# Kernel tuning notes

Hardware: AMD Instinct MI355X
Metric: run time of the kernel (lower is better)

## Reference

```python
import jax, jax.numpy as jnp
import numpy as np

DIM = 1024
NUM_HEADS = 16


def setup_inputs() -> dict:
    key = jax.random.key(0)
    ks = jax.random.split(key, 7)
    B, N, C = 2, 2048, DIM
    s = 1.0 / np.sqrt(C)
    x = jax.random.normal(ks[0], (B, N, C), dtype=jnp.float32)
    Wq = jax.random.normal(ks[1], (C, C), dtype=jnp.float32) * s
    Wk = jax.random.normal(ks[2], (C, C), dtype=jnp.float32) * s
    Wv = jax.random.normal(ks[3], (C, C), dtype=jnp.float32) * s
    bq = jnp.zeros((C,), dtype=jnp.float32)
    bk = jnp.zeros((C,), dtype=jnp.float32)
    bv = jnp.zeros((C,), dtype=jnp.float32)
    return {"x": x, "Wq": Wq, "bq": bq, "Wk": Wk, "bk": bk, "Wv": Wv, "bv": bv}


def reference(x, Wq, bq, Wk, bk, Wv, bv):
    B, N, C = x.shape
    H = NUM_HEADS
    D = C // H
    # Linear projections (torch Linear: x @ W.T + b)
    q = (x @ Wq.T + bq).reshape(B, N, H, D).transpose(0, 2, 1, 3)  # [B,H,N,D]
    k = (x @ Wk.T + bk).reshape(B, N, H, D).transpose(0, 2, 1, 3)
    v = (x @ Wv.T + bv).reshape(B, N, H, D).transpose(0, 2, 1, 3)
    # NOTE: original scales by sqrt(dim)=sqrt(C), not sqrt(head_dim)
    scale = 1.0 / np.sqrt(C).astype(np.float32)
    logits = jnp.einsum('bhnd,bhmd->bhnm', q, k) * scale  # [B,H,N,N]
    attn = jax.nn.softmax(logits, axis=-1)
    out = jnp.einsum('bhnm,bhmd->bhnd', attn, v)  # [B,H,N,D]
    return out.transpose(0, 2, 1, 3).reshape(B, N, C)
```

## Files before the change

kernel.cpp:

```cpp
#include <hip/hip_runtime.h>

typedef __attribute__((ext_vector_type(8))) short bf16x8;
typedef __attribute__((ext_vector_type(4))) float f32x4;
typedef __attribute__((ext_vector_type(16))) float f32x16;
typedef __attribute__((ext_vector_type(8))) unsigned short us8;
typedef unsigned short u16;
typedef unsigned int u32;

__device__ inline u16 f2bf(float f) {
  union { float f; unsigned u; } v; v.f = f;
  unsigned r = v.u + 0x7FFFu + ((v.u >> 16) & 1u);
  return (u16)(r >> 16);
}

__device__ inline u32 cvtpk_bf16(float lo, float hi) {
  u32 r;
  asm volatile("v_cvt_pk_bf16_f32 %0, %1, %2" : "=v"(r) : "v"(lo), "v"(hi));
  return r;
}

__device__ inline void gload_lds16(const void* g, void* l) {
  __builtin_amdgcn_global_load_lds(
      (const __attribute__((address_space(1))) void*)g,
      (__attribute__((address_space(3))) void*)l, 16, 0, 0);
}

__global__ void cvt_all(const float* __restrict__ x, const float* __restrict__ wq,
                        const float* __restrict__ wk, const float* __restrict__ wv,
                        u16* __restrict__ out) {
  int i = (blockIdx.x * blockDim.x + threadIdx.x) * 4;
  const float* src; int off;
  if (i < 4194304)      { src = x;  off = 0; }
  else if (i < 5242880) { src = wq; off = 4194304; }
  else if (i < 6291456) { src = wk; off = 5242880; }
  else                  { src = wv; off = 6291456; }
  float4 v = *reinterpret_cast<const float4*>(src + (i - off));
  ushort4 o;
  o.x = f2bf(v.x); o.y = f2bf(v.y); o.z = f2bf(v.z); o.w = f2bf(v.w);
  *reinterpret_cast<ushort4*>(out + i) = o;
}

__global__ __launch_bounds__(256, 3) void gemm_qkv(
    const u16* __restrict__ X,
    const u16* __restrict__ Wq, const u16* __restrict__ Wk, const u16* __restrict__ Wv,
    const float* __restrict__ bq, const float* __restrict__ bk, const float* __restrict__ bv,
    u16* __restrict__ Oq, u16* __restrict__ Ok, u16* __restrict__ Ov)
{
  constexpr int GK = 1024;
  __shared__ __align__(16) u16 As[128 * 64];
  __shared__ __align__(16) u16 Bs[128 * 64];

  const int z = blockIdx.z;
  const u16* W = (z == 0) ? Wq : (z == 1) ? Wk : Wv;
  const float* bias = (z == 0) ? bq : (z == 1) ? bk : bv;
  u16* O = (z == 0) ? Oq : (z == 1) ? Ok : Ov;
  const float scale = (z == 0) ? (1.4426950408889634f / 32.0f) : 1.0f;

  const int tid = threadIdx.x;
  const int lane = tid & 63, w = tid >> 6;
  const int wm = w >> 1, wn = w & 1;
  const int q = lane & 15, g = lane >> 4;
  const int bm0 = blockIdx.x * 128, bn0 = blockIdx.y * 128;

  int srow[4], sgc[4];
  #pragma unroll
  for (int i = 0; i < 4; ++i) {
    int c = i * 256 + tid;
    srow[i] = c >> 3;
    sgc[i] = (((c & 7) ^ ((c >> 3) & 7)) * 8);
  }

  f32x4 acc[4][4];
  #pragma unroll
  for (int i = 0; i < 4; ++i)
    #pragma unroll
    for (int j = 0; j < 4; ++j) acc[i][j] = (f32x4){0.f, 0.f, 0.f, 0.f};

  for (int k0 = 0; k0 < GK; k0 += 64) {
    #pragma unroll
    for (int i = 0; i < 4; ++i) {
      int c8 = (i * 256 + tid) * 8;
      gload_lds16(&X[(bm0 + srow[i]) * GK + k0 + sgc[i]], &As[c8]);
      gload_lds16(&W[(bn0 + srow[i]) * GK + k0 + sgc[i]], &Bs[c8]);
    }
    __syncthreads();

    #pragma unroll
    for (int kk = 0; kk < 2; ++kk) {
      bf16x8 af[4], bfr[4];
      #pragma unroll
      for (int mi = 0; mi < 4; ++mi) {
        int row = wm * 64 + mi * 16 + q;
        af[mi] = *reinterpret_cast<const bf16x8*>(
            &As[row * 64 + (((kk * 4 + g) ^ (row & 7)) * 8)]);
      }
      #pragma unroll
      for (int ni = 0; ni < 4; ++ni) {
        int row = wn * 64 + ni * 16 + q;
        bfr[ni] = *reinterpret_cast<const bf16x8*>(
            &Bs[row * 64 + (((kk * 4 + g) ^ (row & 7)) * 8)]);
      }
      #pragma unroll
      for (int mi = 0; mi < 4; ++mi)
        #pragma unroll
        for (int ni = 0; ni < 4; ++ni)
          acc[mi][ni] = __builtin_amdgcn_mfma_f32_16x16x32_bf16(af[mi], bfr[ni], acc[mi][ni], 0, 0, 0);
    }
    __syncthreads();
  }

  #pragma unroll
  for (int mi = 0; mi < 4; ++mi) {
    #pragma unroll
    for (int ni = 0; ni < 4; ++ni) {
      int col = bn0 + wn * 64 + ni * 16 + q;
      float bb = bias[col];
      int h = col >> 6, d = col & 63;
      #pragma unroll
      for (int r = 0; r < 4; ++r) {
        int row = bm0 + wm * 64 + mi * 16 + 4 * g + r;
        int b = row >> 11, n = row & 2047;
        float v = (acc[mi][ni][r] + bb) * scale;
        O[(((b << 4) + h) * 2048 + n) * 64 + d] = f2bf(v);
      }
    }
  }
}

__global__ __launch_bounds__(256) void vt_kernel(const u16* __restrict__ V, u16* __restrict__ Vt) {
  __shared__ u16 T[64 * 66];
  const int bh = blockIdx.y, n0 = blockIdx.x * 64;
  const int tid = threadIdx.x;
  #pragma unroll
  for (int i = 0; i < 2; ++i) {
    int c = i * 256 + tid;
    int n = c >> 3, col = (c & 7) * 8;
    us8 v = *reinterpret_cast<const us8*>(&V[(bh * 2048 + n0 + n) * 64 + col]);
    #pragma unroll
    for (int j = 0; j < 8; ++j) T[n * 66 + col + j] = v[j];
  }
  __syncthreads();
  #pragma unroll
  for (int i = 0; i < 2; ++i) {
    int c = i * 256 + tid;
    int d = c >> 3, nc = (c & 7) * 8;
    us8 o;
    #pragma unroll
    for (int j = 0; j < 8; ++j) o[j] = T[(nc + j) * 66 + d];
    *reinterpret_cast<us8*>(&Vt[(bh * 64 + d) * 2048 + n0 + nc]) = o;
  }
}

__global__ __launch_bounds__(512, 4) void attn_kernel(
    const u16* __restrict__ Q, const u16* __restrict__ K, const u16* __restrict__ Vt,
    float* __restrict__ out)
{
  __shared__ __align__(16) u16 smem[32768];
  u16* Kbase = smem;
  u16* Vbase = smem + 16384;

  const int tid = threadIdx.x;
  const int lane = tid & 63, w = tid >> 6;
  const int half = w >> 2, w4 = w & 3;
  const int tid256 = w4 * 64 + lane;
  const int ql = lane & 31, h = lane >> 5, l7 = lane & 7;

  const int lin = blockIdx.x;
  const int xcd = lin & 7, li = lin >> 3;
  const int bh = xcd * 4 + (li >> 4);
  const int b = bh >> 4, hd = bh & 15;
  const int qrow0 = (li & 15) * 128 + w4 * 32;

  const u16* Qp = Q + (bh * 2048 + qrow0 + ql) * 64;
  const u16* Kp = K + (bh * 2048 + half * 1024) * 64;
  const u16* Vp = Vt + bh * 64 * 2048 + half * 1024;

  bf16x8 qf[4];
  #pragma unroll
  for (int ks = 0; ks < 4; ++ks)
    qf[ks] = *reinterpret_cast<const bf16x8*>(Qp + 16 * ks + 8 * h);

  int krow_i[2], kcolb_i[2];
  #pragma unroll
  for (int i = 0; i < 2; ++i) {
    int c = i * 256 + tid256;
    krow_i[i] = c >> 3;
    kcolb_i[i] = 16 * ((c & 7) ^ ((c >> 3) & 7));
  }

  f32x16 o0, o1;
  #pragma unroll
  for (int i = 0; i < 16; ++i) { o0[i] = 0.0f; o1[i] = 0.0f; }
  float lsum = 0.0f;

  u16* Kh = Kbase + half * 8192;
  u16* Vh = Vbase + half * 8192;

  {
    #pragma unroll
    for (int i = 0; i < 2; ++i) {
      gload_lds16((const char*)(Kp + krow_i[i] * 64) + kcolb_i[i],
                  &Kh[i * 2048 + w4 * 512]);
      gload_lds16((const char*)(Vp + krow_i[i] * 2048) + kcolb_i[i],
                  &Vh[i * 2048 + w4 * 512]);
    }
    __syncthreads();
  }

  for (int t = 0; t < 16; ++t) {
    const int cur = t & 1, nxt = cur ^ 1;
    const int kb = t * 64;
    if (t < 15) {
      const int kbn = kb + 64;
      #pragma unroll
      for (int i = 0; i < 2; ++i) {
        gload_lds16((const char*)(Kp + (kbn + krow_i[i]) * 64) + kcolb_i[i],
                    &Kh[nxt * 4096 + i * 2048 + w4 * 512]);
        gload_lds16((const char*)(Vp + krow_i[i] * 2048 + kbn) + kcolb_i[i],
                    &Vh[nxt * 4096 + i * 2048 + w4 * 512]);
      }
    }

    f32x16 p0, p1;
    #pragma unroll
    for (int i = 0; i < 16; ++i) { p0[i] = 0.0f; p1[i] = 0.0f; }
    const u16* kl = Kh + cur * 4096;
    __builtin_amdgcn_s_setprio(1);
    #pragma unroll
    for (int ks = 0; ks < 4; ++ks) {
      int cb = (16 * ks + 8 * h) ^ (l7 << 3);
      bf16x8 kf0 = *reinterpret_cast<const bf16x8*>(kl + ql * 64 + cb);
      p0 = __builtin_amdgcn_mfma_f32_32x32x16_bf16(kf0, qf[ks], p0, 0, 0, 0);
      bf16x8 kf1 = *reinterpret_cast<const bf16x8*>(kl + (32 + ql) * 64 + cb);
      p1 = __builtin_amdgcn_mfma_f32_32x32x16_bf16(kf1, qf[ks], p1, 0, 0, 0);
    }
    __builtin_amdgcn_s_setprio(0);

    #pragma unroll
    for (int i = 0; i < 16; ++i) {
      p0[i] = __builtin_amdgcn_exp2f(p0[i]);
      p1[i] = __builtin_amdgcn_exp2f(p1[i]);
    }
    float sa[8];
    #pragma unroll
    for (int i = 0; i < 8; ++i)
      sa[i] = (p0[i] + p0[i + 8]) + (p1[i] + p1[i + 8]);
    float rs = ((sa[0] + sa[1]) + (sa[2] + sa[3])) + ((sa[4] + sa[5]) + (sa[6] + sa[7]));
    rs += __shfl_xor(rs, 32);
    lsum += rs;

    bf16x8 pf[4];
    {
      union { u32 u[4]; bf16x8 v; } fr;
      u32 a0 = cvtpk_bf16(p0[0], p0[1]),   c0 = cvtpk_bf16(p0[2], p0[3]);
      u32 b0 = cvtpk_bf16(p0[4], p0[5]),   d0 = cvtpk_bf16(p0[6], p0[7]);
      asm volatile("v_permlane32_swap_b32 %0, %1" : "+v"(a0), "+v"(b0));
      asm volatile("v_permlane32_swap_b32 %0, %1" : "+v"(c0), "+v"(d0));
      fr.u[0] = a0; fr.u[1] = c0; fr.u[2] = b0; fr.u[3] = d0;  pf[0] = fr.v;
      u32 a1 = cvtpk_bf16(p0[8], p0[9]),   c1 = cvtpk_bf16(p0[10], p0[11]);
      u32 b1 = cvtpk_bf16(p0[12], p0[13]), d1 = cvtpk_bf16(p0[14], p0[15]);
      asm volatile("v_permlane32_swap_b32 %0, %1" : "+v"(a1), "+v"(b1));
      asm volatile("v_permlane32_swap_b32 %0, %1" : "+v"(c1), "+v"(d1));
      fr.u[0] = a1; fr.u[1] = c1; fr.u[2] = b1; fr.u[3] = d1;  pf[1] = fr.v;
      u32 a2 = cvtpk_bf16(p1[0], p1[1]),   c2 = cvtpk_bf16(p1[2], p1[3]);
      u32 b2 = cvtpk_bf16(p1[4], p1[5]),   d2 = cvtpk_bf16(p1[6], p1[7]);
      asm volatile("v_permlane32_swap_b32 %0, %1" : "+v"(a2), "+v"(b2));
      asm volatile("v_permlane32_swap_b32 %0, %1" : "+v"(c2), "+v"(d2));
      fr.u[0] = a2; fr.u[1] = c2; fr.u[2] = b2; fr.u[3] = d2;  pf[2] = fr.v;
      u32 a3 = cvtpk_bf16(p1[8], p1[9]),   c3 = cvtpk_bf16(p1[10], p1[11]);
      u32 b3 = cvtpk_bf16(p1[12], p1[13]), d3 = cvtpk_bf16(p1[14], p1[15]);
      asm volatile("v_permlane32_swap_b32 %0, %1" : "+v"(a3), "+v"(b3));
      asm volatile("v_permlane32_swap_b32 %0, %1" : "+v"(c3), "+v"(d3));
      fr.u[0] = a3; fr.u[1] = c3; fr.u[2] = b3; fr.u[3] = d3;  pf[3] = fr.v;
    }

    const u16* vl = Vh + cur * 4096;
    __builtin_amdgcn_s_setprio(1);
    #pragma unroll
    for (int f = 0; f < 4; ++f) {
      int cb = (16 * f + 8 * h) ^ (l7 << 3);
      bf16x8 vf0 = *reinterpret_cast<const bf16x8*>(vl + ql * 64 + cb);
      o0 = __builtin_amdgcn_mfma_f32_32x32x16_bf16(vf0, pf[f], o0, 0, 0, 0);
      bf16x8 vf1 = *reinterpret_cast<const bf16x8*>(vl + (32 + ql) * 64 + cb);
      o1 = __builtin_amdgcn_mfma_f32_32x32x16_bf16(vf1, pf[f], o1, 0, 0, 0);
    }
    __builtin_amdgcn_s_setprio(0);

    __syncthreads();
  }

  float* Of = reinterpret_cast<float*>(smem);
  float* Lf = Of + 4 * 64 * 33;
  const int obase = (w4 * 64 + lane) * 33;
  if (half == 1) {
    #pragma unroll
    for (int i = 0; i < 16; ++i) { Of[obase + i] = o0[i]; Of[obase + 16 + i] = o1[i]; }
    Lf[w4 * 64 + lane] = lsum;
  }
  __syncthreads();
  if (half == 0) {
    #pragma unroll
    for (int i = 0; i < 16; ++i) { o0[i] += Of[obase + i]; o1[i] += Of[obase + 16 + i]; }
    lsum += Lf[w4 * 64 + lane];

    float r = 1.0f / lsum;
    float* op = out + ((size_t)(b * 2048 + qrow0 + ql) * 1024 + hd * 64);
    #pragma unroll
    for (int g2 = 0; g2 < 4; ++g2) {
      float4 v0, v1;
      v0.x = o0[4 * g2 + 0] * r; v0.y = o0[4 * g2 + 1] * r;
      v0.z = o0[4 * g2 + 2] * r; v0.w = o0[4 * g2 + 3] * r;
      v1.x = o1[4 * g2 + 0] * r; v1.y = o1[4 * g2 + 1] * r;
      v1.z = o1[4 * g2 + 2] * r; v1.w = o1[4 * g2 + 3] * r;
      *reinterpret_cast<float4*>(op + 8 * g2 + 4 * h)      = v0;
      *reinterpret_cast<float4*>(op + 32 + 8 * g2 + 4 * h) = v1;
    }
  }
}

extern "C" void kernel_launch(void* const* d_in, const int* in_sizes, int n_in,
                              void* d_out, int out_size, void* d_ws, size_t ws_size,
                              hipStream_t stream) {
  const float* x  = (const float*)d_in[0];
  const float* Wq = (const float*)d_in[1];
  const float* bq = (const float*)d_in[2];
  const float* Wk = (const float*)d_in[3];
  const float* bk = (const float*)d_in[4];
  const float* Wv = (const float*)d_in[5];
  const float* bv = (const float*)d_in[6];
  float* out = (float*)d_out;

  u16* ws  = (u16*)d_ws;
  u16* xb  = ws;
  u16* wqb = xb  + 4194304;
  u16* wkb = wqb + 1048576;
  u16* wvb = wkb + 1048576;
  u16* qb  = wvb + 1048576;
  u16* kb  = qb  + 4194304;
  u16* vb  = kb  + 4194304;
  u16* vt  = xb;

  cvt_all<<<7168, 256, 0, stream>>>(x, Wq, Wk, Wv, ws);

  gemm_qkv<<<dim3(32, 8, 3), 256, 0, stream>>>(xb, wqb, wkb, wvb, bq, bk, bv, qb, kb, vb);

  vt_kernel<<<dim3(32, 32), 256, 0, stream>>>(vb, vt);

  attn_kernel<<<512, 512, 0, stream>>>(qb, kb, vt, out);
}
```

Before: 85.28 us.

## Fuse V transpose into QKV GEMM epilogue and prefetch V fragments earlier

The QKV projection epilogue now writes V directly in transposed [b,h,d,n] layout using 4-element vector stores, which removes the separate vt_kernel launch and its extra read/write pass over V. In the attention loop, half of the V fragments are loaded from LDS before the exp/convert stage so their latency overlaps that softmax work. The transposed stores are strided by 2048 across lanes, which may coalesce less well, and the early loads hold extra registers.

```diff
diff --git a/kernel.cpp b/kernel.cpp
--- a/kernel.cpp
+++ b/kernel.cpp
@@ -44,7 +44,7 @@
     const u16* __restrict__ X,
     const u16* __restrict__ Wq, const u16* __restrict__ Wk, const u16* __restrict__ Wv,
     const float* __restrict__ bq, const float* __restrict__ bk, const float* __restrict__ bv,
-    u16* __restrict__ Oq, u16* __restrict__ Ok, u16* __restrict__ Ov)
+    u16* __restrict__ Oq, u16* __restrict__ Ok, u16* __restrict__ Ovt)
 {
   constexpr int GK = 1024;
   __shared__ __align__(16) u16 As[128 * 64];
@@ -53,7 +53,6 @@
   const int z = blockIdx.z;
   const u16* W = (z == 0) ? Wq : (z == 1) ? Wk : Wv;
   const float* bias = (z == 0) ? bq : (z == 1) ? bk : bv;
-  u16* O = (z == 0) ? Oq : (z == 1) ? Ok : Ov;
   const float scale = (z == 0) ? (1.4426950408889634f / 32.0f) : 1.0f;
 
   const int tid = threadIdx.x;
@@ -109,45 +108,42 @@
     __syncthreads();
   }
 
-  #pragma unroll
-  for (int mi = 0; mi < 4; ++mi) {
-    #pragma unroll
-    for (int ni = 0; ni < 4; ++ni) {
-      int col = bn0 + wn * 64 + ni * 16 + q;
-      float bb = bias[col];
-      int h = col >> 6, d = col & 63;
-      #pragma unroll
-      for (int r = 0; r < 4; ++r) {
-        int row = bm0 + wm * 64 + mi * 16 + 4 * g + r;
-        int b = row >> 11, n = row & 2047;
-        float v = (acc[mi][ni][r] + bb) * scale;
-        O[(((b << 4) + h) * 2048 + n) * 64 + d] = f2bf(v);
-      }
-    }
-  }
-}
-
-__global__ __launch_bounds__(256) void vt_kernel(const u16* __restrict__ V, u16* __restrict__ Vt) {
-  __shared__ u16 T[64 * 66];
-  const int bh = blockIdx.y, n0 = blockIdx.x * 64;
-  const int tid = threadIdx.x;
-  #pragma unroll
-  for (int i = 0; i < 2; ++i) {
-    int c = i * 256 + tid;
-    int n = c >> 3, col = (c & 7) * 8;
-    us8 v = *reinterpret_cast<const us8*>(&V[(bh * 2048 + n0 + n) * 64 + col]);
-    #pragma unroll
-    for (int j = 0; j < 8; ++j) T[n * 66 + col + j] = v[j];
-  }
-  __syncthreads();
-  #pragma unroll
-  for (int i = 0; i < 2; ++i) {
-    int c = i * 256 + tid;
-    int d = c >> 3, nc = (c & 7) * 8;
-    us8 o;
-    #pragma unroll
-    for (int j = 0; j < 8; ++j) o[j] = T[(nc + j) * 66 + d];
-    *reinterpret_cast<us8*>(&Vt[(bh * 64 + d) * 2048 + n0 + nc]) = o;
+  if (z == 2) {
+    #pragma unroll
+    for (int mi = 0; mi < 4; ++mi) {
+      #pragma unroll
+      for (int ni = 0; ni < 4; ++ni) {
+        int col = bn0 + wn * 64 + ni * 16 + q;
+        float bb = bias[col];
+        int h = col >> 6, d = col & 63;
+        int row0 = bm0 + wm * 64 + mi * 16 + 4 * g;
+        int b = row0 >> 11, n0 = row0 & 2047;
+        ushort4 o4;
+        o4.x = f2bf(acc[mi][ni][0] + bb);
+        o4.y = f2bf(acc[mi][ni][1] + bb);
+        o4.z = f2bf(acc[mi][ni][2] + bb);
+        o4.w = f2bf(acc[mi][ni][3] + bb);
+        *reinterpret_cast<ushort4*>(&Ovt[(((b << 4) + h) * 64 + d) * 2048 + n0]) = o4;
+      }
+    }
+  } else {
+    u16* O = (z == 0) ? Oq : Ok;
+    #pragma unroll
+    for (int mi = 0; mi < 4; ++mi) {
+      #pragma unroll
+      for (int ni = 0; ni < 4; ++ni) {
+        int col = bn0 + wn * 64 + ni * 16 + q;
+        float bb = bias[col];
+        int h = col >> 6, d = col & 63;
+        #pragma unroll
+        for (int r = 0; r < 4; ++r) {
+          int row = bm0 + wm * 64 + mi * 16 + 4 * g + r;
+          int b = row >> 11, n = row & 2047;
+          float v = (acc[mi][ni][r] + bb) * scale;
+          O[(((b << 4) + h) * 2048 + n) * 64 + d] = f2bf(v);
+        }
+      }
+    }
   }
 }
 
@@ -235,6 +231,14 @@
       p1 = __builtin_amdgcn_mfma_f32_32x32x16_bf16(kf1, qf[ks], p1, 0, 0, 0);
     }
     __builtin_amdgcn_s_setprio(0);
+
+    const u16* vl = Vh + cur * 4096;
+    bf16x8 vf0a[4];
+    #pragma unroll
+    for (int f = 0; f < 4; ++f) {
+      int cb = (16 * f + 8 * h) ^ (l7 << 3);
+      vf0a[f] = *reinterpret_cast<const bf16x8*>(vl + ql * 64 + cb);
+    }
 
     #pragma unroll
     for (int i = 0; i < 16; ++i) {
@@ -274,13 +278,11 @@
       fr.u[0] = a3; fr.u[1] = c3; fr.u[2] = b3; fr.u[3] = d3;  pf[3] = fr.v;
     }
 
-    const u16* vl = Vh + cur * 4096;
     __builtin_amdgcn_s_setprio(1);
     #pragma unroll
     for (int f = 0; f < 4; ++f) {
       int cb = (16 * f + 8 * h) ^ (l7 << 3);
-      bf16x8 vf0 = *reinterpret_cast<const bf16x8*>(vl + ql * 64 + cb);
-      o0 = __builtin_amdgcn_mfma_f32_32x32x16_bf16(vf0, pf[f], o0, 0, 0, 0);
+      o0 = __builtin_amdgcn_mfma_f32_32x32x16_bf16(vf0a[f], pf[f], o0, 0, 0, 0);
       bf16x8 vf1 = *reinterpret_cast<const bf16x8*>(vl + (32 + ql) * 64 + cb);
       o1 = __builtin_amdgcn_mfma_f32_32x32x16_bf16(vf1, pf[f], o1, 0, 0, 0);
     }
@@ -337,14 +339,11 @@
   u16* wvb = wkb + 1048576;
   u16* qb  = wvb + 1048576;
   u16* kb  = qb  + 4194304;
-  u16* vb  = kb  + 4194304;
-  u16* vt  = xb;
+  u16* vt  = kb  + 4194304;
 
   cvt_all<<<7168, 256, 0, stream>>>(x, Wq, Wk, Wv, ws);
 
-  gemm_qkv<<<dim3(32, 8, 3), 256, 0, stream>>>(xb, wqb, wkb, wvb, bq, bk, bv, qb, kb, vb);
-
-  vt_kernel<<<dim3(32, 32), 256, 0, stream>>>(vb, vt);
+  gemm_qkv<<<dim3(32, 8, 3), 256, 0, stream>>>(xb, wqb, wkb, wvb, bq, bk, bv, qb, kb, vt);
 
   attn_kernel<<<512, 512, 0, stream>>>(qb, kb, vt, out);
 }
```

Result: faster. 82.01 us, median of 2 (-3.8%).
